# Kernel tuning notes

Hardware: AMD Instinct MI355X
Metric: run time of the kernel (lower is better)

The kernel has to match this reference:

```python
import jax, jax.numpy as jnp
import numpy as np

DIM = 256
NUM_HEADS = 8
HEAD_DIM = DIM // NUM_HEADS


def rope_sincos(H, W, head_dim, dtype=jnp.float32):
    n = head_dim // 4
    angle = 1.0 / (10000.0 ** jnp.linspace(0.0, 1.0, n))
    angle = jnp.repeat(angle, 2)  # (head_dim//2,)
    ph = jnp.arange(H, dtype=dtype)[:, None] * angle[None, :]  # (H, d/2)
    pw = jnp.arange(W, dtype=dtype)[:, None] * angle[None, :]  # (W, d/2)
    sin_h = jnp.broadcast_to(jnp.sin(ph)[:, None, :], (H, W, 2 * n))
    sin_w = jnp.broadcast_to(jnp.sin(pw)[None, :, :], (H, W, 2 * n))
    cos_h = jnp.broadcast_to(jnp.cos(ph)[:, None, :], (H, W, 2 * n))
    cos_w = jnp.broadcast_to(jnp.cos(pw)[None, :, :], (H, W, 2 * n))
    sin = jnp.concatenate([sin_h, sin_w], -1).reshape(H * W, head_dim)
    cos = jnp.concatenate([cos_h, cos_w], -1).reshape(H * W, head_dim)
    return sin, cos


def rotate_every_two(x):
    x1 = x[..., 0::2]
    x2 = x[..., 1::2]
    return jnp.stack([-x2, x1], axis=-1).reshape(x.shape)


def theta_shift(x, sin, cos):
    return x * cos + rotate_every_two(x) * sin


def conv1x1(x, w, b):
    # x: (B,C,H,W), w: (O,C,1,1)
    return jnp.einsum('bchw,oc->bohw', x, w[:, :, 0, 0]) + b[None, :, None, None]


def depthwise5x5(x, w, b):
    # x: (B,C,H,W), w: (C,1,5,5), groups=C
    y = jax.lax.conv_general_dilated(
        x, w, window_strides=(1, 1), padding=((2, 2), (2, 2)),
        feature_group_count=x.shape[1],
        dimension_numbers=('NCHW', 'OIHW', 'NCHW'))
    return y + b[None, :, None, None]


def setup_inputs() -> dict:
    key = jax.random.key(0)
    ks = jax.random.split(key, 7)
    B, C, H, W = 8, DIM, 64, 64
    x = jax.random.normal(ks[0], (B, C, H, W), dtype=jnp.float32)
    qkvo_w = 0.02 * jax.random.normal(ks[1], (4 * C, C, 1, 1), dtype=jnp.float32)
    qkvo_b = jnp.zeros((4 * C,), dtype=jnp.float32)
    lepe_w = 0.02 * jax.random.normal(ks[2], (C, 1, 5, 5), dtype=jnp.float32)
    lepe_b = jnp.zeros((C,), dtype=jnp.float32)
    proj_w = 0.02 * jax.random.normal(ks[3], (C, C, 1, 1), dtype=jnp.float32)
    proj_b = jnp.zeros((C,), dtype=jnp.float32)
    return {'x': x, 'qkvo_w': qkvo_w, 'qkvo_b': qkvo_b,
            'lepe_w': lepe_w, 'lepe_b': lepe_b,
            'proj_w': proj_w, 'proj_b': proj_b}


def reference(x, qkvo_w, qkvo_b, lepe_w, lepe_b, proj_w, proj_b):
    B, C, H, W = x.shape
    n, d = NUM_HEADS, HEAD_DIM
    L = H * W
    scale = d ** (-0.5)

    sin, cos = rope_sincos(H, W, d, dtype=x.dtype)  # (L, d)

    qkvo = conv1x1(x, qkvo_w, qkvo_b)          # (B, 4C, H, W)
    qkv = qkvo[:, :3 * C]                       # (B, 3C, H, W)
    o = qkvo[:, 3 * C:]                         # (B, C, H, W)
    lepe = depthwise5x5(qkv[:, 2 * C:], lepe_w, lepe_b)  # (B, C, H, W)

    # 'b (m n d) h w -> m b n (h w) d'
    qkv_r = qkv.reshape(B, 3, n, d, H * W).transpose(1, 0, 2, 4, 3)  # (3,B,n,L,d)
    q, k, v = qkv_r[0], qkv_r[1], qkv_r[2]

    q = jax.nn.elu(q) + 1.0
    k = jax.nn.elu(k) + 1.0

    kmean = k.mean(axis=2, keepdims=True)               # (B,n,1,d)
    z = jnp.einsum('bnld,bnmd->bnlm', q, kmean) * scale  # (B,n,L,1)

    q = theta_shift(q, sin, cos)
    k = theta_shift(k, sin, cos)

    c = (scale / L) ** 0.5
    kv = jnp.einsum('bnld,bnle->bnde', k * c, v * c)     # (B,n,d,d)
    vmean = v.mean(axis=2, keepdims=True)                # (B,n,1,d)

    res = jnp.einsum('bnld,bnde->bnle', q, kv) * (1.0 + 1.0 / (z + 1e-6)) - z * vmean
    # 'b n (h w) d -> b (n d) h w'
    res = res.reshape(B, n, H, W, d).transpose(0, 1, 4, 2, 3).reshape(B, C, H, W)
    res = res + lepe
    return conv1x1(res * o, proj_w, proj_b)
```

## Files before the change

### kernel.cpp

```cpp
#include <hip/hip_runtime.h>
#include <math.h>

typedef unsigned short u16;
typedef unsigned int u32;
typedef unsigned long long u64;
typedef __attribute__((ext_vector_type(8))) short short8;
typedef __attribute__((ext_vector_type(4))) float f32x4;
typedef __attribute__((ext_vector_type(16))) float f32x16;

static constexpr float SCALE = 0.17677669529663687f;
static constexpr float C2    = 0.17677669529663687f / 4096.f;

__device__ __forceinline__ float bf2f(u16 u){
  union { u32 i; float f; } v; v.i = ((u32)u) << 16; return v.f;
}
__device__ __forceinline__ u16 f2bf(float f){
  union { float fl; u32 i; } v; v.fl = f;
  u32 r = v.i + 0x7fffu + ((v.i >> 16) & 1u);
  return (u16)(r >> 16);
}
__device__ __forceinline__ float eluP(float x){ return x > 0.f ? x + 1.f : __expf(x); }
__device__ __forceinline__ float rfreq(int j){
  const float t[8] = {1.f, 0.2682695795f, 0.0719685673f, 0.0193069773f,
                      0.0051794747f, 0.0013894955f, 0.0003727594f, 1e-4f};
  return t[j];
}
__device__ __forceinline__ void gload16(const u16* g, u16* l){
  __builtin_amdgcn_global_load_lds(
      (const __attribute__((address_space(1))) u32*)g,
      (__attribute__((address_space(3))) u32*)l, 16, 0, 0);
}

__global__ __launch_bounds__(256) void k_pre(
    const float* __restrict__ x, const float* __restrict__ qw, const float* __restrict__ pw,
    u16* __restrict__ XT, u16* __restrict__ Whi, u16* __restrict__ Wlo,
    u16* __restrict__ Phi, u16* __restrict__ Plo, float* __restrict__ KM0)
{
  if (blockIdx.z < 8){
    __shared__ float t[64][65];
    int l0 = blockIdx.x * 64, c0 = blockIdx.y * 64, b = blockIdx.z;
    const float* xp = x + (((long)b * 256 + c0) << 12) + l0;
    #pragma unroll
    for (int rep = 0; rep < 4; rep++){
      int idx = threadIdx.x + rep * 256;
      int r = idx >> 4, ch = (idx & 15) * 4;
      float4 f = *(const float4*)&xp[((long)r << 12) + ch];
      t[r][ch] = f.x; t[r][ch+1] = f.y; t[r][ch+2] = f.z; t[r][ch+3] = f.w;
    }
    __syncthreads();
    int r2 = threadIdx.x >> 2, c8 = (threadIdx.x & 3) * 16;
    u32 w[8];
    #pragma unroll
    for (int j = 0; j < 8; j++){
      float v0 = t[c8 + 2*j][r2], v1 = t[c8 + 2*j + 1][r2];
      w[j] = (u32)f2bf(v0) | ((u32)f2bf(v1) << 16);
    }
    long ob = (((long)b << 12) << 8) + ((long)(l0 + r2) << 8) + c0 + c8;
    *(uint4*)&XT[ob]     = make_uint4(w[0], w[1], w[2], w[3]);
    *(uint4*)&XT[ob + 8] = make_uint4(w[4], w[5], w[6], w[7]);
  } else {
    int bid = (blockIdx.z - 8) * 256 + blockIdx.y * 64 + blockIdx.x;
    int idx = bid * 256 + threadIdx.x;
    if (idx < 262144){
      float v = qw[idx]; u16 h = f2bf(v);
      Whi[idx] = h; Wlo[idx] = f2bf(v - bf2f(h));
    }
    if (idx < 65536){
      float v = pw[idx]; u16 h = f2bf(v);
      Phi[idx] = h; Plo[idx] = f2bf(v - bf2f(h));
    }
    if (bid == 0){
      #pragma unroll
      for (int i = 0; i < 16; i++) KM0[threadIdx.x + i * 256] = 0.f;
    }
  }
}

__global__ __launch_bounds__(256) void k_gemmA(
    const u16* __restrict__ Whi_, const u16* __restrict__ Wlo_,
    const u16* __restrict__ Bh_,
    const float* __restrict__ bias,
    u16* __restrict__ Q16, u16* __restrict__ K16,
    u16* __restrict__ V16, u16* __restrict__ O16,
    float* __restrict__ KMb, float* __restrict__ VMb)
{
  __shared__ __align__(16) u16 AhS[2][4096];
  __shared__ __align__(16) u16 AlS[2][4096];
  __shared__ __align__(16) u16 BhS[2][4096];
  __shared__ float scs[2][8][64];
  const int tid = threadIdx.x;
  const int nt = blockIdx.x, mt = blockIdx.y, b = blockIdx.z;
  const int m0 = mt * 128, n0 = nt * 128;
  const int wave = tid >> 6, lane = tid & 63;
  const int wm = wave & 1, wn = wave >> 1, qu = lane >> 4, ln = lane & 15;
  const int range = m0 >> 8;

  const u16* bhp = Bh_ + (((long)b << 12) << 8);

  const int l4 = lane >> 2, c4 = lane & 3;
  const int gch = (c4 ^ ((l4 >> 1) & 3)) * 8;
  const int fch = (qu ^ ((ln >> 1) & 3)) * 8;

  auto stage = [&](int buf, int kk){
    #pragma unroll
    for (int t = 0; t < 2; t++){
      int rw = wave * 32 + t * 16;
      int ga = (m0 + rw + l4) * 256 + kk + gch;
      long gb = (long)(n0 + rw + l4) * 256 + kk + gch;
      gload16(&Whi_[ga], &AhS[buf][rw * 32]);
      gload16(&Wlo_[ga], &AlS[buf][rw * 32]);
      gload16(&bhp[gb],  &BhS[buf][rw * 32]);
    }
  };

  f32x4 acc[4][4];
  #pragma unroll
  for (int im = 0; im < 4; im++)
    #pragma unroll
    for (int in = 0; in < 4; in++)
      #pragma unroll
      for (int r = 0; r < 4; r++) acc[im][in][r] = 0.f;

  stage(0, 0);
  if (range == 1){
    #pragma unroll
    for (int r = 0; r < 2; r++){
      int idx = tid + r * 256;
      int jj = idx >> 6, pp = idx & 63;
      float sn, cs; sincosf(rfreq(jj) * (float)pp, &sn, &cs);
      scs[0][jj][pp] = sn; scs[1][jj][pp] = cs;
    }
  }
  __syncthreads();

  int cur = 0;
  #pragma unroll
  for (int ks = 0; ks < 8; ks++){
    if (ks < 7) stage(cur ^ 1, (ks + 1) * 32);
    const u16* Ah = AhS[cur];
    const u16* Al = AlS[cur];
    const u16* Bc = BhS[cur];
    short8 fbh[4];
    #pragma unroll
    for (int in = 0; in < 4; in++){
      int row = wn * 64 + in * 16 + ln;
      fbh[in] = *(const short8*)&Bc[row * 32 + fch];
    }
    #pragma unroll
    for (int im = 0; im < 4; im++){
      int row = wm * 64 + im * 16 + ln;
      short8 fah = *(const short8*)&Ah[row * 32 + fch];
      short8 fal = *(const short8*)&Al[row * 32 + fch];
      #pragma unroll
      for (int in = 0; in < 4; in++){
        acc[im][in] = __builtin_amdgcn_mfma_f32_16x16x32_bf16(fah, fbh[in], acc[im][in], 0, 0, 0);
        acc[im][in] = __builtin_amdgcn_mfma_f32_16x16x32_bf16(fal, fbh[in], acc[im][in], 0, 0, 0);
      }
    }
    if (ks < 7) __syncthreads();
    cur ^= 1;
  }

  u16* dst = (range == 0) ? Q16 : (range == 1) ? K16 : (range == 2) ? V16 : O16;
  #pragma unroll
  for (int im = 0; im < 4; im++){
    const int mb = m0 + wm * 64 + im * 16 + qu * 4;
    float v[4][4];
    #pragma unroll
    for (int r = 0; r < 4; r++){
      float bia = bias[mb + r];
      #pragma unroll
      for (int in = 0; in < 4; in++){
        float t = acc[im][in][r] + bia;
        v[r][in] = (range < 2) ? eluP(t) : t;
      }
    }
    if (range == 1 || range == 2){
      float* mbuf = (range == 1) ? KMb : VMb;
      #pragma unroll
      for (int r = 0; r < 4; r++){
        float s = v[r][0] + v[r][1] + v[r][2] + v[r][3];
        s += __shfl_xor(s, 1); s += __shfl_xor(s, 2);
        s += __shfl_xor(s, 4); s += __shfl_xor(s, 8);
        if (ln == 0) atomicAdd(&mbuf[b * 256 + ((mb + r) & 255)], s);
      }
    }
    if (range == 1){
      const int p0 = (mb & 31) >> 1;
      #pragma unroll
      for (int half = 0; half < 2; half++){
        int p = p0 + half, j = p & 7;
        #pragma unroll
        for (int in = 0; in < 4; in++){
          int n = n0 + wn * 64 + in * 16 + ln;
          int pos = (p < 8) ? (n >> 6) : (n & 63);
          float sn = scs[0][j][pos], cs = scs[1][j][pos];
          float a = v[2*half][in], bb = v[2*half+1][in];
          v[2*half][in]   = a * cs - bb * sn;
          v[2*half+1][in] = bb * cs + a * sn;
        }
      }
    }
    #pragma unroll
    for (int r = 0; r < 4; r++){
      u16* rowp = dst + (((long)b * 256 + ((mb + r) & 255)) << 12);
      #pragma unroll
      for (int in = 0; in < 4; in++){
        int n = n0 + wn * 64 + in * 16 + ln;
        rowp[n] = f2bf(v[r][in]);
      }
    }
  }
}

__global__ __launch_bounds__(256) void k_mid(
    const u16* __restrict__ K16, const u16* __restrict__ V16,
    const float* __restrict__ lw, const float* __restrict__ lb,
    u16* __restrict__ Tb16, float* __restrict__ KVb)
{
  if (blockIdx.y < 256){
    __shared__ float tile[20][68];
    __shared__ float wl[25];
    int ht = blockIdx.x, ch = blockIdx.y, b = blockIdx.z;
    int h0 = ht * 16;
    const u16* vp = V16 + (((long)b * 256 + ch) << 12);
    if (threadIdx.x < 25) wl[threadIdx.x] = lw[ch * 25 + threadIdx.x];
    for (int idx = threadIdx.x; idx < 20 * 68; idx += 256){
      int r = idx / 68, c = idx % 68;
      int gh = h0 + r - 2, gw = c - 2;
      float v = 0.f;
      if (gh >= 0 && gh < 64 && gw >= 0 && gw < 64) v = bf2f(vp[(gh << 6) + gw]);
      tile[r][c] = v;
    }
    __syncthreads();
    const float bia = lb[ch];
    #pragma unroll
    for (int r2 = 0; r2 < 4; r2++){
      int idx = threadIdx.x + r2 * 256;
      int oh = idx >> 6, ow = idx & 63;
      float s = bia;
      #pragma unroll
      for (int i = 0; i < 5; i++)
        #pragma unroll
        for (int j = 0; j < 5; j++) s += tile[oh + i][ow + j] * wl[i * 5 + j];
      Tb16[(((long)b * 256 + ch) << 12) + ((h0 + oh) << 6) + ow] = f2bf(s);
    }
  } else {
    __shared__ float red[4][1024];
    int kvIdx = (blockIdx.y - 256) * 32 + blockIdx.z * 4 + blockIdx.x;
    int n = kvIdx & 7, b = kvIdx >> 3;
    const int tid = threadIdx.x, wave = tid >> 6, lane = tid & 63;
    const u16* kp = K16 + (((long)(b * 256 + n * 32)) << 12);
    const u16* vp = V16 + (((long)(b * 256 + n * 32)) << 12);
    const int m = lane & 31, kh = lane >> 5;
    const long row = ((long)m << 12);

    f32x16 acc;
    #pragma unroll
    for (int r = 0; r < 16; r++) acc[r] = 0.f;
    #pragma unroll 4
    for (int it = 0; it < 64; it++){
      int l = wave * 1024 + it * 16 + kh * 8;
      short8 a  = *(const short8*)&kp[row + l];
      short8 bf = *(const short8*)&vp[row + l];
      acc = __builtin_amdgcn_mfma_f32_32x32x16_bf16(a, bf, acc, 0, 0, 0);
    }
    #pragma unroll
    for (int reg = 0; reg < 16; reg++){
      int rr = (reg & 3) + 8 * (reg >> 2) + 4 * kh;
      red[wave][rr * 32 + m] = acc[reg];
    }
    __syncthreads();
    #pragma unroll
    for (int i = tid; i < 1024; i += 256){
      float s = red[0][i] + red[1][i] + red[2][i] + red[3][i];
      KVb[(((long)b * 8 + n) << 10) + i] = s * C2;
    }
  }
}

__global__ __launch_bounds__(256) void k_res(
    const u16* __restrict__ Q16, const float* __restrict__ KMb,
    const float* __restrict__ KVb, const float* __restrict__ VMb,
    const u16* __restrict__ O16, const u16* __restrict__ Tb16,
    u16* __restrict__ TT16)
{
  __shared__ __align__(16) float kvs[1024];
  __shared__ float scs[2][8][64];
  __shared__ float kms[32], vms[32];
  __shared__ __align__(16) u64 tts[256 * 9];
  const int b = blockIdx.z, n = blockIdx.y, tid = threadIdx.x;
  #pragma unroll
  for (int r = 0; r < 2; r++){
    int idx = tid + r * 256;
    int jj = idx >> 6, pp = idx & 63;
    float sn, cs; sincosf(rfreq(jj) * (float)pp, &sn, &cs);
    scs[0][jj][pp] = sn; scs[1][jj][pp] = cs;
  }
  {
    const float* kv = KVb + (((long)b * 8 + n) << 10);
    #pragma unroll
    for (int r = 0; r < 4; r++) kvs[tid + r * 256] = kv[tid + r * 256];
    if (tid < 32){
      kms[tid] = KMb[b * 256 + n * 32 + tid] * (1.f / 4096.f);
      vms[tid] = VMb[b * 256 + n * 32 + tid] * (1.f / 4096.f);
    }
  }
  __syncthreads();

  const int l0 = blockIdx.x * 256;
  const int l = l0 + tid;
  const long cbase = ((long)(b * 256 + n * 32)) << 12;

  float q[32];
  #pragma unroll
  for (int d = 0; d < 32; d++) q[d] = bf2f(Q16[cbase + ((long)d << 12) + l]);
  float z = 0.f;
  #pragma unroll
  for (int d = 0; d < 32; d++) z += q[d] * kms[d];
  z *= SCALE;
  #pragma unroll
  for (int p = 0; p < 16; p++){
    int pos = (p < 8) ? (l >> 6) : (l & 63);
    float sn = scs[0][p & 7][pos], cs = scs[1][p & 7][pos];
    float q0 = q[2*p], q1 = q[2*p+1];
    q[2*p]   = q0 * cs - q1 * sn;
    q[2*p+1] = q1 * cs + q0 * sn;
  }

  float acc[32];
  #pragma unroll
  for (int e = 0; e < 32; e++) acc[e] = 0.f;
  #pragma unroll 8
  for (int d = 0; d < 32; d++){
    float qd = q[d];
    #pragma unroll
    for (int ec = 0; ec < 8; ec++){
      float4 kvv = *(float4*)&kvs[d * 32 + ec * 4];
      acc[ec*4+0] += qd * kvv.x;
      acc[ec*4+1] += qd * kvv.y;
      acc[ec*4+2] += qd * kvv.z;
      acc[ec*4+3] += qd * kvv.w;
    }
  }

  const float f = 1.f + 1.f / (z + 1e-6f);
  u32 w[16];
  #pragma unroll
  for (int e = 0; e < 32; e++){
    long off = cbase + ((long)e << 12) + l;
    float val = (acc[e] * f - z * vms[e] + bf2f(Tb16[off])) * bf2f(O16[off]);
    u16 h = f2bf(val);
    if (e & 1) w[e >> 1] |= ((u32)h << 16);
    else       w[e >> 1] = h;
  }
  #pragma unroll
  for (int j = 0; j < 8; j++)
    tts[tid * 9 + j] = (u64)w[2*j] | ((u64)w[2*j+1] << 32);
  __syncthreads();
  #pragma unroll
  for (int it = 0; it < 4; it++){
    int row = (tid >> 2) + 64 * it;
    int cc = tid & 3;
    u64 a  = tts[row * 9 + cc * 2];
    u64 bb = tts[row * 9 + cc * 2 + 1];
    long orow = (((long)b << 12) << 8) + ((long)(l0 + row) << 8) + n * 32 + cc * 8;
    *(uint4*)&TT16[orow] = make_uint4((u32)a, (u32)(a >> 32), (u32)bb, (u32)(bb >> 32));
  }
}

__global__ __launch_bounds__(256) void k_gemmP(
    const u16* __restrict__ Phi_, const u16* __restrict__ Plo_,
    const u16* __restrict__ TT16, const float* __restrict__ bias,
    float* __restrict__ out)
{
  __shared__ __align__(16) u16 AhS[2][4096];
  __shared__ __align__(16) u16 AlS[2][4096];
  __shared__ __align__(16) u16 BhS[2][4096];
  const int tid = threadIdx.x;
  const int nt = blockIdx.x, mt = blockIdx.y, b = blockIdx.z;
  const int m0 = mt * 128, n0 = nt * 128;
  const int wave = tid >> 6, lane = tid & 63;
  const int wm = wave & 1, wn = wave >> 1, qu = lane >> 4, ln = lane & 15;

  const u16* bhp = TT16 + (((long)b << 12) << 8);
  const int l4 = lane >> 2, c4 = lane & 3;
  const int gch = (c4 ^ ((l4 >> 1) & 3)) * 8;
  const int fch = (qu ^ ((ln >> 1) & 3)) * 8;

  auto stage = [&](int buf, int kk){
    #pragma unroll
    for (int t = 0; t < 2; t++){
      int rw = wave * 32 + t * 16;
      int ga = (m0 + rw + l4) * 256 + kk + gch;
      long gb = (long)(n0 + rw + l4) * 256 + kk + gch;
      gload16(&Phi_[ga], &AhS[buf][rw * 32]);
      gload16(&Plo_[ga], &AlS[buf][rw * 32]);
      gload16(&bhp[gb],  &BhS[buf][rw * 32]);
    }
  };

  f32x4 acc[4][4];
  #pragma unroll
  for (int im = 0; im < 4; im++)
    #pragma unroll
    for (int in = 0; in < 4; in++)
      #pragma unroll
      for (int r = 0; r < 4; r++) acc[im][in][r] = 0.f;

  stage(0, 0);
  __syncthreads();

  int cur = 0;
  #pragma unroll
  for (int ks = 0; ks < 8; ks++){
    if (ks < 7) stage(cur ^ 1, (ks + 1) * 32);
    const u16* Ah = AhS[cur];
    const u16* Al = AlS[cur];
    const u16* Bc = BhS[cur];
    short8 fbh[4];
    #pragma unroll
    for (int in = 0; in < 4; in++){
      int row = wn * 64 + in * 16 + ln;
      fbh[in] = *(const short8*)&Bc[row * 32 + fch];
    }
    #pragma unroll
    for (int im = 0; im < 4; im++){
      int row = wm * 64 + im * 16 + ln;
      short8 fah = *(const short8*)&Ah[row * 32 + fch];
      short8 fal = *(const short8*)&Al[row * 32 + fch];
      #pragma unroll
      for (int in = 0; in < 4; in++){
        acc[im][in] = __builtin_amdgcn_mfma_f32_16x16x32_bf16(fah, fbh[in], acc[im][in], 0, 0, 0);
        acc[im][in] = __builtin_amdgcn_mfma_f32_16x16x32_bf16(fal, fbh[in], acc[im][in], 0, 0, 0);
      }
    }
    if (ks < 7) __syncthreads();
    cur ^= 1;
  }

  #pragma unroll
  for (int im = 0; im < 4; im++){
    int mbase = m0 + wm * 64 + im * 16 + qu * 4;
    #pragma unroll
    for (int r = 0; r < 4; r++){
      int m = mbase + r;
      float bia = bias[m];
      float* row = out + (((long)b * 256 + m) << 12);
      #pragma unroll
      for (int in = 0; in < 4; in++){
        int n = n0 + wn * 64 + in * 16 + ln;
        row[n] = acc[im][in][r] + bia;
      }
    }
  }
}

extern "C" void kernel_launch(void* const* d_in, const int* in_sizes, int n_in,
                              void* d_out, int out_size, void* d_ws, size_t ws_size,
                              hipStream_t stream)
{
  const float* x  = (const float*)d_in[0];
  const float* qw = (const float*)d_in[1];
  const float* qb = (const float*)d_in[2];
  const float* lw = (const float*)d_in[3];
  const float* lb = (const float*)d_in[4];
  const float* pw = (const float*)d_in[5];
  const float* pb = (const float*)d_in[6];

  u16* W    = (u16*)d_ws;
  u16* Q16  = W;
  u16* K16  = Q16 + 8388608;
  u16* V16  = K16 + 8388608;
  u16* O16  = V16 + 8388608;
  u16* Tb16 = O16 + 8388608;
  u16* XT   = Tb16 + 8388608;
  u16* Whi  = XT + 8388608;
  u16* Wlo  = Whi + 262144;
  u16* Phi  = Wlo + 262144;
  u16* Plo  = Phi + 65536;
  float* KMb = (float*)(Plo + 65536);
  float* VMb = KMb + 2048;
  float* KVb = VMb + 2048;
  size_t total_bytes = (6ull*8388608 + 2*262144 + 2*65536) * 2 + (2048+2048+65536) * 4;
  if (ws_size < total_bytes) return;

  u16* TT16 = XT;

  k_pre<<<dim3(64, 4, 12), 256, 0, stream>>>(x, qw, pw, XT, Whi, Wlo, Phi, Plo, KMb);
  k_gemmA<<<dim3(32, 8, 8), 256, 0, stream>>>(Whi, Wlo, XT, qb,
                                              Q16, K16, V16, O16, KMb, VMb);
  k_mid<<<dim3(4, 258, 8), 256, 0, stream>>>(K16, V16, lw, lb, Tb16, KVb);
  k_res<<<dim3(16, 8, 8), 256, 0, stream>>>(Q16, KMb, KVb, VMb, O16, Tb16, TT16);
  k_gemmP<<<dim3(32, 2, 8), 256, 0, stream>>>(Phi, Plo, TT16, pb, (float*)d_out);
}
```

Baseline: 231.8 us.

## Load low-half weight fragments directly from global and shrink gemmP N tile

In both GEMM kernels the low-order bf16 weight part is no longer staged through LDS; each lane reads its MFMA fragment straight from global/L2 into registers at the start of each k-step. This cuts LDS footprint and the LDS write/read traffic for that operand. gemmP also halves its N tile to 64, doubling the grid to raise occupancy and parallelism. The cost is uncoalesced global fragment reads that depend on cache hits and may expose latency inside the loop, plus more blocks re-reading the weight tiles.

```diff
diff --git a/kernel.cpp b/kernel.cpp
--- a/kernel.cpp
+++ b/kernel.cpp
@@ -85,7 +85,6 @@
     float* __restrict__ KMb, float* __restrict__ VMb)
 {
   __shared__ __align__(16) u16 AhS[2][4096];
-  __shared__ __align__(16) u16 AlS[2][4096];
   __shared__ __align__(16) u16 BhS[2][4096];
   __shared__ float scs[2][8][64];
   const int tid = threadIdx.x;
@@ -101,6 +100,13 @@
   const int gch = (c4 ^ ((l4 >> 1) & 3)) * 8;
   const int fch = (qu ^ ((ln >> 1) & 3)) * 8;
 
+  const u16* ap_l[4];
+  #pragma unroll
+  for (int im = 0; im < 4; im++){
+    int mrow = m0 + wm * 64 + im * 16 + ln;
+    ap_l[im] = Wlo_ + mrow * 256 + qu * 8;
+  }
+
   auto stage = [&](int buf, int kk){
     #pragma unroll
     for (int t = 0; t < 2; t++){
@@ -108,7 +114,6 @@
       int ga = (m0 + rw + l4) * 256 + kk + gch;
       long gb = (long)(n0 + rw + l4) * 256 + kk + gch;
       gload16(&Whi_[ga], &AhS[buf][rw * 32]);
-      gload16(&Wlo_[ga], &AlS[buf][rw * 32]);
       gload16(&bhp[gb],  &BhS[buf][rw * 32]);
     }
   };
@@ -136,9 +141,12 @@
   int cur = 0;
   #pragma unroll
   for (int ks = 0; ks < 8; ks++){
-    if (ks < 7) stage(cur ^ 1, (ks + 1) * 32);
+    const int kk = ks * 32;
+    short8 fl[4];
+    #pragma unroll
+    for (int im = 0; im < 4; im++) fl[im] = *(const short8*)&ap_l[im][kk];
+    if (ks < 7) stage(cur ^ 1, kk + 32);
     const u16* Ah = AhS[cur];
-    const u16* Al = AlS[cur];
     const u16* Bc = BhS[cur];
     short8 fbh[4];
     #pragma unroll
@@ -150,11 +158,10 @@
     for (int im = 0; im < 4; im++){
       int row = wm * 64 + im * 16 + ln;
       short8 fah = *(const short8*)&Ah[row * 32 + fch];
-      short8 fal = *(const short8*)&Al[row * 32 + fch];
       #pragma unroll
       for (int in = 0; in < 4; in++){
         acc[im][in] = __builtin_amdgcn_mfma_f32_16x16x32_bf16(fah, fbh[in], acc[im][in], 0, 0, 0);
-        acc[im][in] = __builtin_amdgcn_mfma_f32_16x16x32_bf16(fal, fbh[in], acc[im][in], 0, 0, 0);
+        acc[im][in] = __builtin_amdgcn_mfma_f32_16x16x32_bf16(fl[im], fbh[in], acc[im][in], 0, 0, 0);
       }
     }
     if (ks < 7) __syncthreads();
@@ -375,11 +382,10 @@
     float* __restrict__ out)
 {
   __shared__ __align__(16) u16 AhS[2][4096];
-  __shared__ __align__(16) u16 AlS[2][4096];
-  __shared__ __align__(16) u16 BhS[2][4096];
+  __shared__ __align__(16) u16 BhS[2][2048];
   const int tid = threadIdx.x;
   const int nt = blockIdx.x, mt = blockIdx.y, b = blockIdx.z;
-  const int m0 = mt * 128, n0 = nt * 128;
+  const int m0 = mt * 128, n0 = nt * 64;
   const int wave = tid >> 6, lane = tid & 63;
   const int wm = wave & 1, wn = wave >> 1, qu = lane >> 4, ln = lane & 15;
 
@@ -388,23 +394,30 @@
   const int gch = (c4 ^ ((l4 >> 1) & 3)) * 8;
   const int fch = (qu ^ ((ln >> 1) & 3)) * 8;
 
+  const u16* ap_l[4];
+  #pragma unroll
+  for (int im = 0; im < 4; im++){
+    int mrow = m0 + wm * 64 + im * 16 + ln;
+    ap_l[im] = Plo_ + mrow * 256 + qu * 8;
+  }
+
   auto stage = [&](int buf, int kk){
     #pragma unroll
     for (int t = 0; t < 2; t++){
       int rw = wave * 32 + t * 16;
       int ga = (m0 + rw + l4) * 256 + kk + gch;
-      long gb = (long)(n0 + rw + l4) * 256 + kk + gch;
       gload16(&Phi_[ga], &AhS[buf][rw * 32]);
-      gload16(&Plo_[ga], &AlS[buf][rw * 32]);
-      gload16(&bhp[gb],  &BhS[buf][rw * 32]);
-    }
+    }
+    int rwb = wave * 16;
+    long gb = (long)(n0 + rwb + l4) * 256 + kk + gch;
+    gload16(&bhp[gb], &BhS[buf][rwb * 32]);
   };
 
-  f32x4 acc[4][4];
+  f32x4 acc[4][2];
   #pragma unroll
   for (int im = 0; im < 4; im++)
     #pragma unroll
-    for (int in = 0; in < 4; in++)
+    for (int in = 0; in < 2; in++)
       #pragma unroll
       for (int r = 0; r < 4; r++) acc[im][in][r] = 0.f;
 
@@ -414,25 +427,27 @@
   int cur = 0;
   #pragma unroll
   for (int ks = 0; ks < 8; ks++){
-    if (ks < 7) stage(cur ^ 1, (ks + 1) * 32);
+    const int kk = ks * 32;
+    short8 fl[4];
+    #pragma unroll
+    for (int im = 0; im < 4; im++) fl[im] = *(const short8*)&ap_l[im][kk];
+    if (ks < 7) stage(cur ^ 1, kk + 32);
     const u16* Ah = AhS[cur];
-    const u16* Al = AlS[cur];
     const u16* Bc = BhS[cur];
-    short8 fbh[4];
-    #pragma unroll
-    for (int in = 0; in < 4; in++){
-      int row = wn * 64 + in * 16 + ln;
+    short8 fbh[2];
+    #pragma unroll
+    for (int in = 0; in < 2; in++){
+      int row = wn * 32 + in * 16 + ln;
       fbh[in] = *(const short8*)&Bc[row * 32 + fch];
     }
     #pragma unroll
     for (int im = 0; im < 4; im++){
       int row = wm * 64 + im * 16 + ln;
       short8 fah = *(const short8*)&Ah[row * 32 + fch];
-      short8 fal = *(const short8*)&Al[row * 32 + fch];
-      #pragma unroll
-      for (int in = 0; in < 4; in++){
+      #pragma unroll
+      for (int in = 0; in < 2; in++){
         acc[im][in] = __builtin_amdgcn_mfma_f32_16x16x32_bf16(fah, fbh[in], acc[im][in], 0, 0, 0);
-        acc[im][in] = __builtin_amdgcn_mfma_f32_16x16x32_bf16(fal, fbh[in], acc[im][in], 0, 0, 0);
+        acc[im][in] = __builtin_amdgcn_mfma_f32_16x16x32_bf16(fl[im], fbh[in], acc[im][in], 0, 0, 0);
       }
     }
     if (ks < 7) __syncthreads();
@@ -448,8 +463,8 @@
       float bia = bias[m];
       float* row = out + (((long)b * 256 + m) << 12);
       #pragma unroll
-      for (int in = 0; in < 4; in++){
-        int n = n0 + wn * 64 + in * 16 + ln;
+      for (int in = 0; in < 2; in++){
+        int n = n0 + wn * 32 + in * 16 + ln;
         row[n] = acc[im][in][r] + bia;
       }
     }
@@ -492,5 +507,5 @@
                                               Q16, K16, V16, O16, KMb, VMb);
   k_mid<<<dim3(4, 258, 8), 256, 0, stream>>>(K16, V16, lw, lb, Tb16, KVb);
   k_res<<<dim3(16, 8, 8), 256, 0, stream>>>(Q16, KMb, KVb, VMb, O16, Tb16, TT16);
-  k_gemmP<<<dim3(32, 2, 8), 256, 0, stream>>>(Phi, Plo, TT16, pb, (float*)d_out);
-}
+  k_gemmP<<<dim3(64, 2, 8), 256, 0, stream>>>(Phi, Plo, TT16, pb, (float*)d_out);
+}
```

After: 256.2 us. 10.5% more time.

## Triple-buffer LDS staging in QKVO and projection GEMMs with vmcnt waits

Applied to the files above, without the earlier changes.

Both GEMM kernels move from double-buffered to triple-buffered LDS staging, prefetching two k-steps ahead. The full __syncthreads is replaced with a partial s_waitcnt vmcnt(6) plus s_barrier, so only the oldest stage's loads must land before compute. This is meant to hide more global-to-LDS latency behind MFMA work. In exchange, shared memory per block rises by half, which may lower occupancy, and correctness now depends on exact hand-counted vmcnt values and the direct-to-LDS load semantics.

```diff
diff --git a/kernel.cpp b/kernel.cpp
--- a/kernel.cpp
+++ b/kernel.cpp
@@ -84,9 +84,9 @@
     u16* __restrict__ V16, u16* __restrict__ O16,
     float* __restrict__ KMb, float* __restrict__ VMb)
 {
-  __shared__ __align__(16) u16 AhS[2][4096];
-  __shared__ __align__(16) u16 AlS[2][4096];
-  __shared__ __align__(16) u16 BhS[2][4096];
+  __shared__ __align__(16) u16 AhS[3][4096];
+  __shared__ __align__(16) u16 AlS[3][4096];
+  __shared__ __align__(16) u16 BhS[3][4096];
   __shared__ float scs[2][8][64];
   const int tid = threadIdx.x;
   const int nt = blockIdx.x, mt = blockIdx.y, b = blockIdx.z;
@@ -122,6 +122,7 @@
       for (int r = 0; r < 4; r++) acc[im][in][r] = 0.f;
 
   stage(0, 0);
+  stage(1, 32);
   if (range == 1){
     #pragma unroll
     for (int r = 0; r < 2; r++){
@@ -131,15 +132,18 @@
       scs[0][jj][pp] = sn; scs[1][jj][pp] = cs;
     }
   }
-  __syncthreads();
-
-  int cur = 0;
+  asm volatile("s_waitcnt lgkmcnt(0)" ::: "memory");
+
   #pragma unroll
   for (int ks = 0; ks < 8; ks++){
-    if (ks < 7) stage(cur ^ 1, (ks + 1) * 32);
-    const u16* Ah = AhS[cur];
-    const u16* Al = AlS[cur];
-    const u16* Bc = BhS[cur];
+    if (ks < 7) asm volatile("s_waitcnt vmcnt(6)" ::: "memory");
+    else        asm volatile("s_waitcnt vmcnt(0)" ::: "memory");
+    __builtin_amdgcn_s_barrier();
+    __builtin_amdgcn_sched_barrier(0);
+    if (ks < 6) stage((ks + 2) % 3, (ks + 2) * 32);
+    const u16* Ah = AhS[ks % 3];
+    const u16* Al = AlS[ks % 3];
+    const u16* Bc = BhS[ks % 3];
     short8 fbh[4];
     #pragma unroll
     for (int in = 0; in < 4; in++){
@@ -157,8 +161,6 @@
         acc[im][in] = __builtin_amdgcn_mfma_f32_16x16x32_bf16(fal, fbh[in], acc[im][in], 0, 0, 0);
       }
     }
-    if (ks < 7) __syncthreads();
-    cur ^= 1;
   }
 
   u16* dst = (range == 0) ? Q16 : (range == 1) ? K16 : (range == 2) ? V16 : O16;
@@ -374,9 +376,9 @@
     const u16* __restrict__ TT16, const float* __restrict__ bias,
     float* __restrict__ out)
 {
-  __shared__ __align__(16) u16 AhS[2][4096];
-  __shared__ __align__(16) u16 AlS[2][4096];
-  __shared__ __align__(16) u16 BhS[2][4096];
+  __shared__ __align__(16) u16 AhS[3][4096];
+  __shared__ __align__(16) u16 AlS[3][4096];
+  __shared__ __align__(16) u16 BhS[3][4096];
   const int tid = threadIdx.x;
   const int nt = blockIdx.x, mt = blockIdx.y, b = blockIdx.z;
   const int m0 = mt * 128, n0 = nt * 128;
@@ -409,15 +411,18 @@
       for (int r = 0; r < 4; r++) acc[im][in][r] = 0.f;
 
   stage(0, 0);
-  __syncthreads();
-
-  int cur = 0;
+  stage(1, 32);
+
   #pragma unroll
   for (int ks = 0; ks < 8; ks++){
-    if (ks < 7) stage(cur ^ 1, (ks + 1) * 32);
-    const u16* Ah = AhS[cur];
-    const u16* Al = AlS[cur];
-    const u16* Bc = BhS[cur];
+    if (ks < 7) asm volatile("s_waitcnt vmcnt(6)" ::: "memory");
+    else        asm volatile("s_waitcnt vmcnt(0)" ::: "memory");
+    __builtin_amdgcn_s_barrier();
+    __builtin_amdgcn_sched_barrier(0);
+    if (ks < 6) stage((ks + 2) % 3, (ks + 2) * 32);
+    const u16* Ah = AhS[ks % 3];
+    const u16* Al = AlS[ks % 3];
+    const u16* Bc = BhS[ks % 3];
     short8 fbh[4];
     #pragma unroll
     for (int in = 0; in < 4; in++){
@@ -435,8 +440,6 @@
         acc[im][in] = __builtin_amdgcn_mfma_f32_16x16x32_bf16(fal, fbh[in], acc[im][in], 0, 0, 0);
       }
     }
-    if (ks < 7) __syncthreads();
-    cur ^= 1;
   }
 
   #pragma unroll
```

Result: slower. 237.9 us (+2.6%).
